# Kernel tuning notes

Hardware: AMD Instinct MI355X
Metric: run time of the kernel (lower is better)

Reference implementation:

```python
import jax, jax.numpy as jnp
import numpy as np

D = 1024
H = 16
DH = D // H
NEG = -10000000.0


def setup_inputs() -> dict:
    key = jax.random.key(0)
    ks = jax.random.split(key, 12)
    B, L = 2, 2048
    sc = 0.02
    inp = {
        "q": jax.random.normal(ks[0], (B, L, D), jnp.float32),
        "k": jax.random.normal(ks[1], (B, L, D), jnp.float32),
        "v": jax.random.normal(ks[2], (B, L, D), jnp.float32),
        "attention_mask": jax.random.randint(ks[3], (B, L, L), 0, 2) == 1,
        "head_mask": jnp.ones((1, 1, 1), jnp.float32),
        "Wq": sc * jax.random.normal(ks[4], (D, D), jnp.float32),
        "bq": jnp.zeros((D,), jnp.float32),
        "Wk": sc * jax.random.normal(ks[5], (D, D), jnp.float32),
        "bk": jnp.zeros((D,), jnp.float32),
        "Wv": sc * jax.random.normal(ks[6], (D, D), jnp.float32),
        "bv": jnp.zeros((D,), jnp.float32),
        "Wo": sc * jax.random.normal(ks[7], (D, D), jnp.float32),
        "bo": jnp.zeros((D,), jnp.float32),
    }
    return inp


def reference(q, k, v, attention_mask, head_mask, Wq, bq, Wk, bk, Wv, bv, Wo, bo):
    B, Lq, _ = q.shape
    Lk = k.shape[1]
    # QKV projections (nn.Linear: x @ W.T + b), split into heads
    qh = (q @ Wq.T + bq).reshape(B, Lq, H, DH)  # [B,Lq,H,dh]
    kh = (k @ Wk.T + bk).reshape(B, Lk, H, DH)
    vh = (v @ Wv.T + bv).reshape(B, Lk, H, DH)
    # scores [B,H,Lq,Lk], scaled by 1/sqrt(dh)
    scores = jnp.einsum("bihd,bjhd->bhij", qh, kh) / jnp.sqrt(jnp.float32(DH))
    scores = jnp.where(attention_mask[:, None, :, :], NEG, scores)
    probs = jax.nn.softmax(scores, axis=-1)
    probs = probs * head_mask  # broadcastable head mask (dropout is identity in eval)
    ctx = jnp.einsum("bhij,bjhd->bihd", probs, vh).reshape(B, Lq, D)
    # output linear + residual (Add_and_LN with with_lN=False, eval dropout)
    out = ctx @ Wo.T + bo + q
    return out
```

## Files before the change

### kernel.cpp

```cpp
#include <hip/hip_runtime.h>

typedef unsigned short u16;
typedef unsigned long long u64;
typedef __attribute__((ext_vector_type(4))) float f32x4;
typedef __attribute__((ext_vector_type(8))) short s16x8;
typedef __attribute__((ext_vector_type(4))) short s16x4;
typedef __attribute__((ext_vector_type(4))) unsigned int u32x4;
typedef __attribute__((ext_vector_type(2))) unsigned int u32x2;

#define LDS_LOAD16(gp, lp) __builtin_amdgcn_global_load_lds( \
    (__attribute__((address_space(1))) void*)(gp), \
    (__attribute__((address_space(3))) void*)(lp), 16, 0, 0)

#define MFMA16 __builtin_amdgcn_mfma_f32_16x16x32_bf16

constexpr float L2E = 1.44269504088896340736f;

__device__ __forceinline__ u16 f2bf(float x) {
  unsigned u = __float_as_uint(x);
  u += 0x7FFF + ((u >> 16) & 1);
  return (u16)(u >> 16);
}

__device__ __forceinline__ unsigned cvtpk_bf16(float lo, float hi) {
  unsigned r;
  asm("v_cvt_pk_bf16_f32 %0, %1, %2" : "=v"(r) : "v"(lo), "v"(hi));
  return r;
}

struct ConvArgs {
  const float* src[7];
  u16* dst[7];
  int n4[7];
  float scale[7];
};

__global__ __launch_bounds__(256) void convert_many(ConvArgs a) {
  const int arr = blockIdx.y;
  const f32x4* src = (const f32x4*)a.src[arr];
  u16* dst = a.dst[arr];
  const int n4 = a.n4[arr];
  const float sc = a.scale[arr];
  const int stride = gridDim.x * blockDim.x;
  for (int i = blockIdx.x * blockDim.x + threadIdx.x; i < n4; i += stride) {
    f32x4 v = src[i];
    s16x4 o;
#pragma unroll
    for (int j = 0; j < 4; ++j) o[j] = (short)f2bf(v[j] * sc);
    *(s16x4*)(dst + (size_t)i * 4) = o;
  }
}

__global__ __launch_bounds__(256) void mask_to_bits(const unsigned int* __restrict__ m32,
                                                    unsigned long long* __restrict__ bits,
                                                    int n) {
  const int i = blockIdx.x * blockDim.x + threadIdx.x;
  const int lane = threadIdx.x & 63;
  unsigned probe = m32[lane];
  bool bytemode = __any(probe > 1u);
  bool v;
  if (bytemode) v = ((const unsigned char*)m32)[i] != 0;
  else          v = m32[i] != 0;
  unsigned long long b = __ballot(v);
  if (lane == 0) bits[i >> 6] = b;
}

struct QkvArgsB {
  const u16* A[3];
  const u16* B[3];
  const float* bias[3];
  float bscale[3];
  u16* C[3];
};

__global__ __launch_bounds__(256) void gemm_qkv_bf(QkvArgsB a) {
  const int z = blockIdx.z;
  const u16* __restrict__ A = a.A[z];
  const u16* __restrict__ B = a.B[z];
  const float* __restrict__ bias = a.bias[z];
  const float bscale = a.bscale[z];
  u16* __restrict__ C = a.C[z];

  __shared__ u16 As[2][4096];
  __shared__ u16 Bs[2][4096];
  const int tid = threadIdx.x;
  const int lane = tid & 63;
  const int wave = tid >> 6;
  const int g = lane >> 4, c = lane & 15;
  const int g4 = g * 4;
  const int bx = blockIdx.x;
  const int row0 = (((bx & 7) << 2) | (bx >> 3)) * 128;
  const int col0 = blockIdx.y * 128;
  const int wr = (wave >> 1) * 64, wc = (wave & 1) * 64;

  f32x4 acc[4][4] = {};

#define STAGE_QKV(p_, k0_) { _Pragma("unroll") \
    for (int i = 0; i < 2; ++i) { \
      int e = (i * 256 + tid) * 8; \
      LDS_LOAD16(A + (size_t)(row0 + (e >> 5)) * 1024 + (k0_) + (e & 31), As[p_] + e); \
      LDS_LOAD16(B + (size_t)(col0 + (e >> 5)) * 1024 + (k0_) + (e & 31), Bs[p_] + e); } }

  STAGE_QKV(0, 0);
  __syncthreads();

  for (int s = 0; s < 32; ++s) {
    const int p = s & 1;
    if (s < 31) STAGE_QKV(p ^ 1, (s + 1) * 32);
    s16x8 af[4], bf[4];
#pragma unroll
    for (int m = 0; m < 4; ++m) af[m] = *(const s16x8*)(As[p] + (wr + m * 16 + c) * 32 + g * 8);
#pragma unroll
    for (int n = 0; n < 4; ++n) bf[n] = *(const s16x8*)(Bs[p] + (wc + n * 16 + c) * 32 + g * 8);
#pragma unroll
    for (int m = 0; m < 4; ++m)
#pragma unroll
      for (int n = 0; n < 4; ++n)
        acc[m][n] = MFMA16(bf[n], af[m], acc[m][n], 0, 0, 0);
    __syncthreads();
  }

  f32x4 bv[4];
#pragma unroll
  for (int n = 0; n < 4; ++n) {
    bv[n] = *(const f32x4*)(bias + col0 + wc + n * 16 + g4);
#pragma unroll
    for (int r = 0; r < 4; ++r) bv[n][r] *= bscale;
  }
#pragma unroll
  for (int m = 0; m < 4; ++m)
#pragma unroll
    for (int n = 0; n < 4; ++n) {
      s16x4 o;
#pragma unroll
      for (int r = 0; r < 4; ++r) o[r] = (short)f2bf(acc[m][n][r] + bv[n][r]);
      *(s16x4*)(C + (size_t)(row0 + wr + m * 16 + c) * 1024 + col0 + wc + n * 16 + g4) = o;
    }
}

struct QkvArgsF {
  const float* A[3];
  const u16* B[3];
  const float* bias[3];
  float bscale[3];
  u16* C[3];
};

__global__ __launch_bounds__(256) void gemm_qkv_f32(QkvArgsF a) {
  const int z = blockIdx.z;
  const float* __restrict__ A = a.A[z];
  const u16* __restrict__ B = a.B[z];
  const float* __restrict__ bias = a.bias[z];
  const float bscale = a.bscale[z];
  u16* __restrict__ C = a.C[z];

  __shared__ u16 As[2][4096];
  __shared__ u16 Bs[2][4096];
  const int tid = threadIdx.x;
  const int lane = tid & 63;
  const int wave = tid >> 6;
  const int g = lane >> 4, c = lane & 15;
  const int g4 = g * 4;
  const int row0 = blockIdx.x * 128;
  const int col0 = blockIdx.y * 128;
  const int wr = (wave >> 1) * 64, wc = (wave & 1) * 64;
  const int ra = tid >> 2;
  const int cca = (tid & 3) * 8;

  f32x4 acc[4][4] = {};
  f32x4 ar[2][2];
#pragma unroll
  for (int i = 0; i < 2; ++i) {
    ar[i][0] = *(const f32x4*)(A + (size_t)(row0 + i * 64 + ra) * 1024 + cca);
    ar[i][1] = *(const f32x4*)(A + (size_t)(row0 + i * 64 + ra) * 1024 + cca + 4);
  }

  for (int s = 0; s < 32; ++s) {
    const int p = s & 1;
    const int k0 = s * 32;
#pragma unroll
    for (int i = 0; i < 2; ++i) {
      unsigned w0 = cvtpk_bf16(ar[i][0][0], ar[i][0][1]);
      unsigned w1 = cvtpk_bf16(ar[i][0][2], ar[i][0][3]);
      unsigned w2 = cvtpk_bf16(ar[i][1][0], ar[i][1][1]);
      unsigned w3 = cvtpk_bf16(ar[i][1][2], ar[i][1][3]);
      union { u32x4 u; s16x8 v; } w;
      w.u = (u32x4){w0, w1, w2, w3};
      *(s16x8*)(As[p] + (i * 256 + tid) * 8) = w.v;
    }
    if (s < 31) {
#pragma unroll
      for (int i = 0; i < 2; ++i) {
        ar[i][0] = *(const f32x4*)(A + (size_t)(row0 + i * 64 + ra) * 1024 + k0 + 32 + cca);
        ar[i][1] = *(const f32x4*)(A + (size_t)(row0 + i * 64 + ra) * 1024 + k0 + 32 + cca + 4);
      }
    }
#pragma unroll
    for (int i = 0; i < 2; ++i) {
      int e = (i * 256 + tid) * 8;
      LDS_LOAD16(B + (size_t)(col0 + (e >> 5)) * 1024 + k0 + (e & 31), Bs[p] + e);
    }
    __syncthreads();

    s16x8 af[4], bf[4];
#pragma unroll
    for (int m = 0; m < 4; ++m) af[m] = *(const s16x8*)(As[p] + (wr + m * 16 + c) * 32 + g * 8);
#pragma unroll
    for (int n = 0; n < 4; ++n) bf[n] = *(const s16x8*)(Bs[p] + (wc + n * 16 + c) * 32 + g * 8);
#pragma unroll
    for (int m = 0; m < 4; ++m)
#pragma unroll
      for (int n = 0; n < 4; ++n)
        acc[m][n] = MFMA16(bf[n], af[m], acc[m][n], 0, 0, 0);
  }

  f32x4 bv[4];
#pragma unroll
  for (int n = 0; n < 4; ++n) {
    bv[n] = *(const f32x4*)(bias + col0 + wc + n * 16 + g4);
#pragma unroll
    for (int r = 0; r < 4; ++r) bv[n][r] *= bscale;
  }
#pragma unroll
  for (int m = 0; m < 4; ++m)
#pragma unroll
    for (int n = 0; n < 4; ++n) {
      s16x4 o;
#pragma unroll
      for (int r = 0; r < 4; ++r) o[r] = (short)f2bf(acc[m][n][r] + bv[n][r]);
      *(s16x4*)(C + (size_t)(row0 + wr + m * 16 + c) * 1024 + col0 + wc + n * 16 + g4) = o;
    }
}

__global__ __launch_bounds__(256) void gemm_out(const u16* __restrict__ A,
                                                const u16* __restrict__ B,
                                                const float* __restrict__ bias,
                                                const float* __restrict__ resid,
                                                float* __restrict__ C) {
  __shared__ u16 As[2][2048];
  __shared__ u16 Bs[2][4096];
  const int tid = threadIdx.x;
  const int lane = tid & 63;
  const int wave = tid >> 6;
  const int g = lane >> 4, c = lane & 15;
  const int g4 = g * 4;
  const int bx = blockIdx.x;
  const int row0 = (((bx & 7) << 3) | (bx >> 3)) * 64;
  const int col0 = blockIdx.y * 128;
  const int wr = (wave >> 1) * 32, wc = (wave & 1) * 64;

  f32x4 acc[2][4] = {};

#define STAGE_OUT(p_, k0_) { \
    LDS_LOAD16(A + (size_t)(row0 + (tid >> 2)) * 1024 + (k0_) + (tid & 3) * 8, As[p_] + tid * 8); \
    _Pragma("unroll") \
    for (int i = 0; i < 2; ++i) { \
      int e = (i * 256 + tid) * 8; \
      LDS_LOAD16(B + (size_t)(col0 + (e >> 5)) * 1024 + (k0_) + (e & 31), Bs[p_] + e); } }

  STAGE_OUT(0, 0);
  __syncthreads();

  for (int s = 0; s < 32; ++s) {
    const int p = s & 1;
    if (s < 31) STAGE_OUT(p ^ 1, (s + 1) * 32);
    s16x8 af[2], bf[4];
#pragma unroll
    for (int m = 0; m < 2; ++m) af[m] = *(const s16x8*)(As[p] + (wr + m * 16 + c) * 32 + g * 8);
#pragma unroll
    for (int n = 0; n < 4; ++n) bf[n] = *(const s16x8*)(Bs[p] + (wc + n * 16 + c) * 32 + g * 8);
#pragma unroll
    for (int m = 0; m < 2; ++m)
#pragma unroll
      for (int n = 0; n < 4; ++n)
        acc[m][n] = MFMA16(bf[n], af[m], acc[m][n], 0, 0, 0);
    __syncthreads();
  }

  f32x4 bv[4];
#pragma unroll
  for (int n = 0; n < 4; ++n) bv[n] = *(const f32x4*)(bias + col0 + wc + n * 16 + g4);
#pragma unroll
  for (int m = 0; m < 2; ++m)
#pragma unroll
    for (int n = 0; n < 4; ++n) {
      size_t off = (size_t)(row0 + wr + m * 16 + c) * 1024 + col0 + wc + n * 16 + g4;
      f32x4 rv = *(const f32x4*)(resid + off);
      f32x4 o;
#pragma unroll
      for (int r = 0; r < 4; ++r) o[r] = acc[m][n][r] + bv[n][r] + rv[r];
      *(f32x4*)(C + off) = o;
    }
}

constexpr float NEGV = -10000000.0f;

__global__ __launch_bounds__(256) void attn_kernel(const u16* __restrict__ Qh,
                                                   const u16* __restrict__ Kh,
                                                   const u16* __restrict__ Vh,
                                                   const u64* __restrict__ mbits,
                                                   const float* __restrict__ head_mask,
                                                   u16* __restrict__ ctx) {
  __shared__ u16 Ks[2][4096];
  __shared__ u16 Vt[2][64 * 72];

  const int tid = threadIdx.x;
  const int lane = tid & 63;
  const int wave = tid >> 6;
  const int g = lane >> 4, c = lane & 15;
  const int g4 = g * 4;
  const int wid = (blockIdx.x & 7) * 64 + (blockIdx.x >> 3);
  const int qt = wid & 15;
  const int bh = wid >> 4;
  const int b = bh >> 4;
  const int h = bh & 15;
  const size_t rowbase = (size_t)b * 2048;
  const int D = 1024;

  s16x8 qf[2][2];
#pragma unroll
  for (int s = 0; s < 2; ++s) {
    const int qrow = qt * 128 + s * 64 + wave * 16 + c;
#pragma unroll
    for (int ks = 0; ks < 2; ++ks)
      qf[s][ks] = *(const s16x8*)(Qh + (rowbase + qrow) * D + h * 64 + ks * 32 + g * 8);
  }

  f32x4 accO[2][4] = {};
  float srun[2] = {0.f, 0.f};

  const u64* mrow0 = mbits + (rowbase + qt * 128 + 0 * 64 + wave * 16 + c) * 32;
  const u64* mrow1 = mbits + (rowbase + qt * 128 + 1 * 64 + wave * 16 + c) * 32;

  const int kkK = tid & 63;
  const int aV = tid >> 3;
  const int sV = tid & 7;
  const int dcV = sV * 8;
  const int colV = (2 * aV) ^ (8 * sV);

  const u16* Kbase = Kh + rowbase * D + h * 64;
  const u16* Vbase = Vh + rowbase * D + h * 64;

  s16x8 kreg[2], vreg[2];
#define LOADKV(kb_) { \
    kreg[0] = *(const s16x8*)(Kbase + (size_t)((kb_) + kkK) * D + wave * 8); \
    kreg[1] = *(const s16x8*)(Kbase + (size_t)((kb_) + kkK) * D + (4 + wave) * 8); \
    vreg[0] = *(const s16x8*)(Vbase + (size_t)((kb_) + 2 * aV) * D + dcV); \
    vreg[1] = *(const s16x8*)(Vbase + (size_t)((kb_) + 2 * aV + 1) * D + dcV); }
#define WRITEKV(p_) { \
    *(s16x8*)(Ks[p_] + tid * 8) = kreg[0]; \
    *(s16x8*)(Ks[p_] + 2048 + tid * 8) = kreg[1]; \
    _Pragma("unroll") \
    for (int j = 0; j < 8; ++j) { \
      unsigned pk = (unsigned)(u16)vreg[0][j] | ((unsigned)(u16)vreg[1][j] << 16); \
      *(unsigned*)(Vt[p_] + (dcV + j) * 72 + colV) = pk; } }

  LOADKV(0);
  WRITEKV(0);
  LOADKV(64);
  __syncthreads();

  for (int it = 0; it < 32; ++it) {
    const int p = it & 1;
    if (it < 31) WRITEKV(p ^ 1);
    if (it < 30) LOADKV((it + 2) * 64);

    f32x4 accS[2][4];
#pragma unroll
    for (int t = 0; t < 4; ++t) {
      s16x8 kf0 = *(const s16x8*)(Ks[p] + ((0 + g) * 64 + t * 16 + c) * 8);
      s16x8 kf1 = *(const s16x8*)(Ks[p] + ((4 + g) * 64 + t * 16 + c) * 8);
      f32x4 z0 = {0.f, 0.f, 0.f, 0.f};
      z0 = MFMA16(kf0, qf[0][0], z0, 0, 0, 0);
      accS[0][t] = MFMA16(kf1, qf[0][1], z0, 0, 0, 0);
      f32x4 z1 = {0.f, 0.f, 0.f, 0.f};
      z1 = MFMA16(kf0, qf[1][0], z1, 0, 0, 0);
      accS[1][t] = MFMA16(kf1, qf[1][1], z1, 0, 0, 0);
    }

    s16x8 pa[2][2];
#pragma unroll
    for (int s = 0; s < 2; ++s) {
      u64 mw = (s == 0 ? mrow0 : mrow1)[it];
      u64 sh = mw >> g4;
      unsigned mlo = (unsigned)sh, mhi = (unsigned)(sh >> 32);
      float sp = 0.f;
      unsigned pk0[4], pk1[4];
#pragma unroll
      for (int t = 0; t < 4; ++t) {
        unsigned msrc = (t < 2) ? mlo : mhi;
#pragma unroll
        for (int r = 0; r < 4; ++r) {
          float sv = accS[s][t][r];
          if ((msrc >> ((t & 1) * 16 + r)) & 1) sv = NEGV;
          float pv;
          asm("v_exp_f32 %0, %1" : "=v"(pv) : "v"(sv));
          accS[s][t][r] = pv;
          sp += pv;
        }
        pk0[t] = cvtpk_bf16(accS[s][t][0], accS[s][t][1]);
        pk1[t] = cvtpk_bf16(accS[s][t][2], accS[s][t][3]);
      }
      srun[s] += sp;
#pragma unroll
      for (int ks = 0; ks < 2; ++ks) {
        union { u32x4 u; s16x8 v; } w;
        w.u = (u32x4){pk0[2 * ks], pk1[2 * ks], pk0[2 * ks + 1], pk1[2 * ks + 1]};
        pa[s][ks] = w.v;
      }
    }

#pragma unroll
    for (int d0 = 0; d0 < 4; ++d0) {
      const int dd = d0 * 16 + c;
      const int sw8 = (d0 * 2 + (c >> 3)) * 8;
#pragma unroll
      for (int ks = 0; ks < 2; ++ks) {
        const int base = ks * 32 + g4;
        u32x2 lo = *(const u32x2*)(Vt[p] + dd * 72 + (base ^ sw8));
        u32x2 hi = *(const u32x2*)(Vt[p] + dd * 72 + ((base + 16) ^ sw8));
        union { u32x4 u; s16x8 v; } w;
        w.u = (u32x4){lo[0], lo[1], hi[0], hi[1]};
        accO[0][d0] = MFMA16(w.v, pa[0][ks], accO[0][d0], 0, 0, 0);
        accO[1][d0] = MFMA16(w.v, pa[1][ks], accO[1][d0], 0, 0, 0);
      }
    }
    __syncthreads();
  }

  const float hm = head_mask[0];
#pragma unroll
  for (int s = 0; s < 2; ++s) {
    float tot = srun[s];
    tot += __shfl_xor(tot, 16, 64);
    tot += __shfl_xor(tot, 32, 64);
    float inv = hm / tot;
    const int qrow = qt * 128 + s * 64 + wave * 16 + c;
#pragma unroll
    for (int d0 = 0; d0 < 4; ++d0) {
      s16x4 o;
#pragma unroll
      for (int r = 0; r < 4; ++r) o[r] = (short)f2bf(accO[s][d0][r] * inv);
      *(s16x4*)(ctx + (rowbase + qrow) * D + h * 64 + d0 * 16 + g4) = o;
    }
  }
}

extern "C" void kernel_launch(void* const* d_in, const int* in_sizes, int n_in,
                              void* d_out, int out_size, void* d_ws, size_t ws_size,
                              hipStream_t stream) {
  const float* q  = (const float*)d_in[0];
  const float* k  = (const float*)d_in[1];
  const float* v  = (const float*)d_in[2];
  const void*  am = d_in[3];
  const float* hm = (const float*)d_in[4];
  const float* Wq = (const float*)d_in[5];
  const float* bq = (const float*)d_in[6];
  const float* Wk = (const float*)d_in[7];
  const float* bk = (const float*)d_in[8];
  const float* Wv = (const float*)d_in[9];
  const float* bv = (const float*)d_in[10];
  const float* Wo = (const float*)d_in[11];
  const float* bo = (const float*)d_in[12];

  char* ws = (char*)d_ws;
  const size_t MB = 1024 * 1024;
  const bool big = ws_size >= 58 * MB;

  if (big) {
    u16* qb  = (u16*)(ws + 0 * MB);
    u16* kb  = (u16*)(ws + 8 * MB);
    u16* vb  = (u16*)(ws + 16 * MB);
    u16* wqb = (u16*)(ws + 24 * MB);
    u16* wkb = (u16*)(ws + 26 * MB);
    u16* wvb = (u16*)(ws + 28 * MB);
    u16* wob = (u16*)(ws + 30 * MB);
    u16* Qh  = (u16*)(ws + 32 * MB);
    u16* Kh  = (u16*)(ws + 40 * MB);
    u16* Vh  = (u16*)(ws + 48 * MB);
    unsigned long long* mbits = (unsigned long long*)(ws + 56 * MB);
    u16* ctx = qb;

    ConvArgs ca;
    ca.src[0] = q;  ca.dst[0] = qb;  ca.n4[0] = 1048576; ca.scale[0] = 1.f;
    ca.src[1] = k;  ca.dst[1] = kb;  ca.n4[1] = 1048576; ca.scale[1] = 1.f;
    ca.src[2] = v;  ca.dst[2] = vb;  ca.n4[2] = 1048576; ca.scale[2] = 1.f;
    ca.src[3] = Wq; ca.dst[3] = wqb; ca.n4[3] = 262144;  ca.scale[3] = 0.125f * L2E;
    ca.src[4] = Wk; ca.dst[4] = wkb; ca.n4[4] = 262144;  ca.scale[4] = 1.f;
    ca.src[5] = Wv; ca.dst[5] = wvb; ca.n4[5] = 262144;  ca.scale[5] = 1.f;
    ca.src[6] = Wo; ca.dst[6] = wob; ca.n4[6] = 262144;  ca.scale[6] = 1.f;
    convert_many<<<dim3(512, 7), 256, 0, stream>>>(ca);

    mask_to_bits<<<32768, 256, 0, stream>>>((const unsigned int*)am, mbits, 8388608);

    QkvArgsB ga;
    ga.A[0] = qb; ga.B[0] = wqb; ga.bias[0] = bq; ga.bscale[0] = 0.125f * L2E; ga.C[0] = Qh;
    ga.A[1] = kb; ga.B[1] = wkb; ga.bias[1] = bk; ga.bscale[1] = 1.f;          ga.C[1] = Kh;
    ga.A[2] = vb; ga.B[2] = wvb; ga.bias[2] = bv; ga.bscale[2] = 1.f;          ga.C[2] = Vh;
    gemm_qkv_bf<<<dim3(32, 8, 3), 256, 0, stream>>>(ga);

    attn_kernel<<<512, 256, 0, stream>>>(Qh, Kh, Vh, mbits, hm, ctx);

    gemm_out<<<dim3(64, 8), 256, 0, stream>>>(ctx, wob, bo, q, (float*)d_out);
  } else {
    u16* Qh  = (u16*)(ws + 0 * MB);
    u16* Kh  = (u16*)(ws + 8 * MB);
    u16* Vh  = (u16*)(ws + 16 * MB);
    u16* wqb = (u16*)(ws + 24 * MB);
    u16* wkb = (u16*)(ws + 26 * MB);
    u16* wvb = (u16*)(ws + 28 * MB);
    u16* wob = (u16*)(ws + 30 * MB);
    unsigned long long* mbits = (unsigned long long*)(ws + 32 * MB);
    u16* ctx = (u16*)(ws + 33 * MB);

    ConvArgs ca;
    ca.src[0] = Wq; ca.dst[0] = wqb; ca.n4[0] = 262144; ca.scale[0] = 0.125f * L2E;
    ca.src[1] = Wk; ca.dst[1] = wkb; ca.n4[1] = 262144; ca.scale[1] = 1.f;
    ca.src[2] = Wv; ca.dst[2] = wvb; ca.n4[2] = 262144; ca.scale[2] = 1.f;
    ca.src[3] = Wo; ca.dst[3] = wob; ca.n4[3] = 262144; ca.scale[3] = 1.f;
    convert_many<<<dim3(256, 4), 256, 0, stream>>>(ca);

    mask_to_bits<<<32768, 256, 0, stream>>>((const unsigned int*)am, mbits, 8388608);

    QkvArgsF ga;
    ga.A[0] = q; ga.B[0] = wqb; ga.bias[0] = bq; ga.bscale[0] = 0.125f * L2E; ga.C[0] = Qh;
    ga.A[1] = k; ga.B[1] = wkb; ga.bias[1] = bk; ga.bscale[1] = 1.f;          ga.C[1] = Kh;
    ga.A[2] = v; ga.B[2] = wvb; ga.bias[2] = bv; ga.bscale[2] = 1.f;          ga.C[2] = Vh;
    gemm_qkv_f32<<<dim3(32, 8, 3), 256, 0, stream>>>(ga);

    attn_kernel<<<512, 256, 0, stream>>>(Qh, Kh, Vh, mbits, hm, ctx);

    gemm_out<<<dim3(64, 8), 256, 0, stream>>>(ctx, wob, bo, q, (float*)d_out);
  }
}
```

Before: 162.9 us.

## Triple-buffer GEMM LDS staging with vmcnt waits; raise wave priority around attention MFMAs

The QKV and output projection GEMMs move from double-buffered to triple-buffered LDS staging. Loads are issued two stages ahead, each iteration waits with explicit s_waitcnt vmcnt counts, and a single barrier per iteration replaces the two __syncthreads. This is meant to hide global-to-LDS latency better, at the cost of more LDS per block, which may lower occupancy. The attention kernel also raises wave priority around its MFMA blocks so matrix work is favoured over the softmax/exp sections of other waves.

```diff
diff --git a/kernel.cpp b/kernel.cpp
--- a/kernel.cpp
+++ b/kernel.cpp
@@ -81,8 +81,8 @@
   const float bscale = a.bscale[z];
   u16* __restrict__ C = a.C[z];
 
-  __shared__ u16 As[2][4096];
-  __shared__ u16 Bs[2][4096];
+  __shared__ u16 As[3][4096];
+  __shared__ u16 Bs[3][4096];
   const int tid = threadIdx.x;
   const int lane = tid & 63;
   const int wave = tid >> 6;
@@ -102,11 +102,18 @@
       LDS_LOAD16(B + (size_t)(col0 + (e >> 5)) * 1024 + (k0_) + (e & 31), Bs[p_] + e); } }
 
   STAGE_QKV(0, 0);
-  __syncthreads();
+  STAGE_QKV(1, 32);
 
   for (int s = 0; s < 32; ++s) {
-    const int p = s & 1;
-    if (s < 31) STAGE_QKV(p ^ 1, (s + 1) * 32);
+    const int p = s % 3;
+    if (s == 31) asm volatile("s_waitcnt vmcnt(0)" ::: "memory");
+    else         asm volatile("s_waitcnt vmcnt(4)" ::: "memory");
+    __builtin_amdgcn_s_barrier();
+    __builtin_amdgcn_sched_barrier(0);
+    if (s + 2 < 32) {
+      const int np = (s + 2) % 3;
+      STAGE_QKV(np, (s + 2) * 32);
+    }
     s16x8 af[4], bf[4];
 #pragma unroll
     for (int m = 0; m < 4; ++m) af[m] = *(const s16x8*)(As[p] + (wr + m * 16 + c) * 32 + g * 8);
@@ -117,7 +124,6 @@
 #pragma unroll
       for (int n = 0; n < 4; ++n)
         acc[m][n] = MFMA16(bf[n], af[m], acc[m][n], 0, 0, 0);
-    __syncthreads();
   }
 
   f32x4 bv[4];
@@ -237,8 +243,8 @@
                                                 const float* __restrict__ bias,
                                                 const float* __restrict__ resid,
                                                 float* __restrict__ C) {
-  __shared__ u16 As[2][2048];
-  __shared__ u16 Bs[2][4096];
+  __shared__ u16 As[3][2048];
+  __shared__ u16 Bs[3][4096];
   const int tid = threadIdx.x;
   const int lane = tid & 63;
   const int wave = tid >> 6;
@@ -259,11 +265,18 @@
       LDS_LOAD16(B + (size_t)(col0 + (e >> 5)) * 1024 + (k0_) + (e & 31), Bs[p_] + e); } }
 
   STAGE_OUT(0, 0);
-  __syncthreads();
+  STAGE_OUT(1, 32);
 
   for (int s = 0; s < 32; ++s) {
-    const int p = s & 1;
-    if (s < 31) STAGE_OUT(p ^ 1, (s + 1) * 32);
+    const int p = s % 3;
+    if (s == 31) asm volatile("s_waitcnt vmcnt(0)" ::: "memory");
+    else         asm volatile("s_waitcnt vmcnt(3)" ::: "memory");
+    __builtin_amdgcn_s_barrier();
+    __builtin_amdgcn_sched_barrier(0);
+    if (s + 2 < 32) {
+      const int np = (s + 2) % 3;
+      STAGE_OUT(np, (s + 2) * 32);
+    }
     s16x8 af[2], bf[4];
 #pragma unroll
     for (int m = 0; m < 2; ++m) af[m] = *(const s16x8*)(As[p] + (wr + m * 16 + c) * 32 + g * 8);
@@ -274,7 +287,6 @@
 #pragma unroll
       for (int n = 0; n < 4; ++n)
         acc[m][n] = MFMA16(bf[n], af[m], acc[m][n], 0, 0, 0);
-    __syncthreads();
   }
 
   f32x4 bv[4];
@@ -366,6 +378,7 @@
     if (it < 30) LOADKV((it + 2) * 64);
 
     f32x4 accS[2][4];
+    __builtin_amdgcn_s_setprio(1);
 #pragma unroll
     for (int t = 0; t < 4; ++t) {
       s16x8 kf0 = *(const s16x8*)(Ks[p] + ((0 + g) * 64 + t * 16 + c) * 8);
@@ -377,6 +390,7 @@
       z1 = MFMA16(kf0, qf[1][0], z1, 0, 0, 0);
       accS[1][t] = MFMA16(kf1, qf[1][1], z1, 0, 0, 0);
     }
+    __builtin_amdgcn_s_setprio(0);
 
     s16x8 pa[2][2];
 #pragma unroll
@@ -410,6 +424,7 @@
       }
     }
 
+    __builtin_amdgcn_s_setprio(1);
 #pragma unroll
     for (int d0 = 0; d0 < 4; ++d0) {
       const int dd = d0 * 16 + c;
@@ -425,6 +440,7 @@
         accO[1][d0] = MFMA16(w.v, pa[1][ks], accO[1][d0], 0, 0, 0);
       }
     }
+    __builtin_amdgcn_s_setprio(0);
     __syncthreads();
   }
 
```

Measured after the change: 158.8 us. 1.03x faster.
